# Optimization experiments

Measured on AMD Instinct MI355X. Metric: run time of the kernel, lower is better.

## Reference

```python
import jax, jax.numpy as jnp
import numpy as np

V, E, H, A, B, S = 32000, 1024, 1024, 1024, 64, 512

def setup_inputs() -> dict:
    key = jax.random.key(0)
    ks = jax.random.split(key, 20)
    sc = lambda d: 1.0 / np.sqrt(d)
    return {
        "x": jax.random.randint(ks[0], (B,), 0, V),
        "encoder_outputs": jax.random.normal(ks[1], (S, B, H), jnp.float32),
        "h0": jax.random.normal(ks[2], (1, B, H), jnp.float32),
        "c0": jax.random.normal(ks[3], (1, B, H), jnp.float32),
        "Wa": jax.random.normal(ks[4], (A, H), jnp.float32) * sc(H),
        "b_wa": jnp.zeros((A,), jnp.float32),
        "Ua": jax.random.normal(ks[5], (A, H), jnp.float32) * sc(H),
        "b_ua": jnp.zeros((A,), jnp.float32),
        "va": jax.random.normal(ks[6], (1, A), jnp.float32) * sc(A),
        "b_va": jnp.zeros((1,), jnp.float32),
        "emb": jax.random.normal(ks[7], (V, E), jnp.float32) * 0.02,
        "W_ih": jax.random.normal(ks[8], (4 * H, E + H), jnp.float32) * sc(E + H),
        "W_hh": jax.random.normal(ks[9], (4 * H, H), jnp.float32) * sc(H),
        "b_ih": jnp.zeros((4 * H,), jnp.float32),
        "b_hh": jnp.zeros((4 * H,), jnp.float32),
        "W_clf": jax.random.normal(ks[10], (V, H), jnp.float32) * sc(H),
        "b_clf": jnp.zeros((V,), jnp.float32),
    }

def reference(x, encoder_outputs, h0, c0, Wa, b_wa, Ua, b_ua, va, b_va, emb,
              W_ih, W_hh, b_ih, b_hh, W_clf, b_clf):
    # Bahdanau additive attention: scores over time (axis 0)
    tmp1 = jnp.einsum('lbh,ah->lba', h0, Wa) + b_wa            # [1,B,A]
    tmp2 = jnp.einsum('sbh,ah->sba', encoder_outputs, Ua) + b_ua  # [S,B,A]
    scores = jnp.einsum('sba,oa->sbo', jnp.tanh(tmp1 + tmp2), va) + b_va  # [S,B,1]
    w = jax.nn.softmax(scores, axis=0)                          # softmax over S
    ctx = jnp.einsum('sb,sbh->bh', w[..., 0], encoder_outputs)  # [B,H]
    # embed token, concat with context
    inp = jnp.concatenate([emb[x], ctx], axis=-1)               # [B,E+H]
    # single LSTM step (PyTorch gate order i,f,g,o)
    gates = inp @ W_ih.T + b_ih + h0[0] @ W_hh.T + b_hh         # [B,4H]
    i, f, g, o = jnp.split(gates, 4, axis=-1)
    c1 = jax.nn.sigmoid(f) * c0[0] + jax.nn.sigmoid(i) * jnp.tanh(g)
    h1 = jax.nn.sigmoid(o) * jnp.tanh(c1)
    logits = h1 @ W_clf.T + b_clf                               # [B,V]
    return jax.nn.log_softmax(logits, axis=-1)[None]            # [1,B,V]
```

## Files before the change

kernel.cpp:

```cpp
#include <hip/hip_runtime.h>
#include <hip/hip_bf16.h>
#include <math.h>

typedef unsigned short u16;
typedef unsigned int u32;
typedef __attribute__((ext_vector_type(4))) float f32x4;
typedef __attribute__((ext_vector_type(8))) short s16x8;
typedef __attribute__((ext_vector_type(8))) unsigned short u16x8;

#define DEV __device__ __forceinline__


DEV u16 f2bf(float f) {
    union { float f; u32 u; } x{f};
    return (u16)((x.u + 0x7FFFu + ((x.u >> 16) & 1u)) >> 16);
}
DEV float bf2f(u16 h) {
    union { u32 u; float f; } x;
    x.u = ((u32)h) << 16;
    return x.f;
}
DEV float sigm(float x) { return 1.0f / (1.0f + __expf(-x)); }
DEV float tanh_f(float x) {
    float c = fminf(fmaxf(x, -9.0f), 9.0f);
    float e = __expf(2.0f * c);
    return (e - 1.0f) / (e + 1.0f);
}

#define GLL16(g, l) __builtin_amdgcn_global_load_lds( \
    (const __attribute__((address_space(1))) u32*)(g), \
    (__attribute__((address_space(3))) u32*)(l), 16, 0, 0)

__global__ __launch_bounds__(256) void kprepcvt(
    const float* __restrict__ enc, const float* __restrict__ Ua,
    const float* __restrict__ h0, u16* __restrict__ encbf,
    u16* __restrict__ Uabf, u16* __restrict__ h0bf, float* __restrict__ scores)
{
    int bid = blockIdx.x, t = threadIdx.x;
    if (bid < 16384) {
        int i = bid * 256 + t;
        float4 f0 = ((const float4*)enc)[i * 2];
        float4 f1 = ((const float4*)enc)[i * 2 + 1];
        u16x8 o = {f2bf(f0.x), f2bf(f0.y), f2bf(f0.z), f2bf(f0.w),
                   f2bf(f1.x), f2bf(f1.y), f2bf(f1.z), f2bf(f1.w)};
        ((u16x8*)encbf)[i] = o;
    } else if (bid < 16400) {
        int i = (bid - 16384) * 2048 + t * 8;
        *(float4*)(scores + i) = (float4){0.f, 0.f, 0.f, 0.f};
        *(float4*)(scores + i + 4) = (float4){0.f, 0.f, 0.f, 0.f};
    } else if (bid < 16912) {
        int i = (bid - 16400) * 256 + t;
        float4 f0 = ((const float4*)Ua)[i * 2];
        float4 f1 = ((const float4*)Ua)[i * 2 + 1];
        u16x8 o = {f2bf(f0.x), f2bf(f0.y), f2bf(f0.z), f2bf(f0.w),
                   f2bf(f1.x), f2bf(f1.y), f2bf(f1.z), f2bf(f1.w)};
        ((u16x8*)Uabf)[i] = o;
    } else {
        int i = (bid - 16912) * 256 + t;
        float4 f0 = ((const float4*)h0)[i * 2];
        float4 f1 = ((const float4*)h0)[i * 2 + 1];
        u16x8 o = {f2bf(f0.x), f2bf(f0.y), f2bf(f0.z), f2bf(f0.w),
                   f2bf(f1.x), f2bf(f1.y), f2bf(f1.z), f2bf(f1.w)};
        ((u16x8*)h0bf)[i] = o;
    }
}


template<int F0>
DEV void mmq(f32x4 (&acc)[8][4], const s16x8 (&af)[2][2], const s16x8 (&bfrag)[4][2]) {
#pragma unroll
    for (int f = 0; f < 2; f++)
#pragma unroll
        for (int j = 0; j < 4; j++) {
            acc[F0 + f][j] = __builtin_amdgcn_mfma_f32_16x16x32_bf16(af[f][0], bfrag[j][0], acc[F0 + f][j], 0, 0, 0);
            acc[F0 + f][j] = __builtin_amdgcn_mfma_f32_16x16x32_bf16(af[f][1], bfrag[j][1], acc[F0 + f][j], 0, 0, 0);
        }
}

__global__ __launch_bounds__(512, 1) void kscores256v2(
    const u16* __restrict__ encbf, const u16* __restrict__ Uabf,
    const float* __restrict__ tmp1c, const float* __restrict__ va,
    float* __restrict__ scores)
{
    __shared__ __align__(16) u16 shm[65536];

    int wg  = blockIdx.x;
    int lin = (wg & 7) * 64 + (wg >> 3);
    int mt  = lin >> 2, nt = lin & 3;

    int t = threadIdx.x;
    int wid = t >> 6, lane = t & 63;
    int wm = wid >> 2, wn = wid & 3;
    int lr = lane & 15, lg = lane >> 4;

    f32x4 acc[8][4];
#pragma unroll
    for (int i = 0; i < 8; i++)
#pragma unroll
        for (int j = 0; j < 4; j++) acc[i][j] = (f32x4){0.f, 0.f, 0.f, 0.f};

    int srow = t >> 3;
    int sq8  = ((t & 7) ^ (srow & 7)) * 8;
    const u16* asrcb = encbf + (size_t)(mt * 256 + srow) * 1024 + sq8;
    const u16* bsrcb = Uabf + (size_t)(nt * 256 + srow) * 1024 + sq8;

#define STG_A(SE, RB, KO) GLL16(asrcb + (size_t)(RB) * 1024 + (KO), shm + (SE) + (RB) * 64 + t * 8)
#define STG_B(SE, RB, KO) GLL16(bsrcb + (size_t)(RB) * 1024 + (KO), shm + (SE) + 16384 + (RB) * 64 + t * 8)

    const u16* Abase = shm + (wm * 128 + lr) * 64;
    const u16* Bbase = shm + 16384 + (wn * 64 + lr) * 64;
    int xor8 = (lr & 7) * 8;
    int o0 = (lg * 8) ^ xor8;
    int o1 = (32 + lg * 8) ^ xor8;

    s16x8 af[2][2], bfrag[4][2];

#define RD_A2(F0, AB) { \
    af[0][0] = *(const s16x8*)((AB) + (F0) * 1024 + o0); \
    af[0][1] = *(const s16x8*)((AB) + (F0) * 1024 + o1); \
    af[1][0] = *(const s16x8*)((AB) + (F0 + 1) * 1024 + o0); \
    af[1][1] = *(const s16x8*)((AB) + (F0 + 1) * 1024 + o1); }

#define MM(F0) \
    __builtin_amdgcn_s_setprio(1); \
    mmq<F0>(acc, af, bfrag); \
    __builtin_amdgcn_s_setprio(0);

#define BAR() \
    __builtin_amdgcn_s_barrier(); \
    __builtin_amdgcn_sched_barrier(0);

    STG_B(0, 0, 0);  STG_B(0, 64, 0);  STG_B(0, 128, 0); STG_B(0, 192, 0);
    STG_A(0, 0, 0);  STG_A(0, 128, 0); STG_A(0, 64, 0);  STG_A(0, 192, 0);
    STG_B(32768, 0, 64);  STG_B(32768, 64, 64);
    STG_B(32768, 128, 64); STG_B(32768, 192, 64);
    STG_A(32768, 0, 64);  STG_A(32768, 128, 64);
    asm volatile("s_waitcnt vmcnt(6)" ::: "memory");
    BAR();

#define TILE_BODY(T, SB, SBX, SAH, STP2, WC) { \
    int kA = (T) * 64 + 128; \
    int kH = (T) * 64 + 64; \
    const u16* Ab = Abase + (SB); \
    const u16* Bb = Bbase + (SB); \
     \
    if (SAH) { STG_A((SBX), 64, kH); STG_A((SBX), 192, kH); } \
    _Pragma("unroll") \
    for (int j = 0; j < 4; j++) { \
        bfrag[j][0] = *(const s16x8*)(Bb + j * 1024 + o0); \
        bfrag[j][1] = *(const s16x8*)(Bb + j * 1024 + o1); \
    } \
    RD_A2(0, Ab); \
    MM(0); \
    BAR();                       \
     \
    if (STP2) { STG_B((SB), 0, kA); STG_B((SB), 64, kA); } \
    RD_A2(2, Ab); \
    MM(2); \
    __builtin_amdgcn_sched_barrier(0); \
     \
    if (STP2) { STG_B((SB), 128, kA); STG_B((SB), 192, kA); } \
    RD_A2(4, Ab); \
    MM(4); \
    BAR();                       \
     \
    if (STP2) { STG_A((SB), 0, kA); STG_A((SB), 128, kA); } \
    RD_A2(6, Ab); \
    if ((WC) == 6) { asm volatile("s_waitcnt vmcnt(6)" ::: "memory"); } \
    else if ((WC) == 0) { asm volatile("s_waitcnt vmcnt(0)" ::: "memory"); } \
    MM(6); \
    BAR();                       \
}

    for (int tt = 0; tt < 7; tt++) {
        int T0 = tt * 2;
        TILE_BODY(T0, 0, 32768, 1, 1, 6);
        TILE_BODY(T0 + 1, 32768, 0, 1, 1, 6);
    }
    TILE_BODY(14, 0, 32768, 1, 0, 0);
    TILE_BODY(15, 32768, 0, 0, 0, -1);

    float* ltmp = (float*)shm;
#pragma unroll
    for (int i = 0; i < 8; i++) {
        int idx = t + i * 512;
        int row = idx >> 6, c4 = idx & 63;
        float4 v = *(const float4*)(tmp1c + row * 1024 + nt * 256 + c4 * 4);
        *(float4*)(ltmp + row * 260 + c4 * 4) = v;
    }
    __syncthreads();

    float vaj[4];
#pragma unroll
    for (int j = 0; j < 4; j++) vaj[j] = va[nt * 256 + wn * 64 + j * 16 + lr];

#pragma unroll
    for (int fi = 0; fi < 8; fi++) {
        float rs[4] = {0.f, 0.f, 0.f, 0.f};
#pragma unroll
        for (int j = 0; j < 4; j++) {
            int ac = wn * 64 + j * 16 + lr;
#pragma unroll
            for (int r = 0; r < 4; r++) {
                int b = (fi * 16 + lg * 4 + r) & 63;
                rs[r] += vaj[j] * tanh_f(acc[fi][j][r] + ltmp[b * 260 + ac]);
            }
        }
#pragma unroll
        for (int m = 1; m < 16; m <<= 1)
#pragma unroll
            for (int r = 0; r < 4; r++) rs[r] += __shfl_xor(rs[r], m, 64);
        if (lr == 0) {
            int mrow = mt * 256 + wm * 128 + fi * 16 + lg * 4;
#pragma unroll
            for (int r = 0; r < 4; r++) atomicAdd(&scores[mrow + r], rs[r]);
        }
    }
#undef STG_A
#undef STG_B
#undef RD_A2
#undef MM
#undef BAR
#undef TILE_BODY
}

__global__ __launch_bounds__(256) void kskinny(
    const u16* __restrict__ Abf, int Ktot,
    const float* __restrict__ B1, int K1,
    const float* __restrict__ B2,
    float* __restrict__ Cout, int N, int klen)
{
    __shared__ u16 As[64 * 40];
    __shared__ u16 Bs[128 * 40];

    int nt = blockIdx.x, p = blockIdx.y;
    int t = threadIdx.x;
    int wid = t >> 6, lane = t & 63;
    int lr = lane & 15, lg = lane >> 4;
    int K2 = Ktot - K1;

    f32x4 acc[4][2];
#pragma unroll
    for (int i = 0; i < 4; i++)
#pragma unroll
        for (int j = 0; j < 2; j++) acc[i][j] = (f32x4){0.f, 0.f, 0.f, 0.f};

    int arow = t >> 2, aq = t & 3;
    const u16* ap = Abf + (size_t)arow * Ktot + aq * 8;
    u16* asw = &As[arow * 40 + aq * 8];

    int brow = t >> 1, bhalf = t & 1;
    int n = nt * 128 + brow;
    u16* bsw = &Bs[brow * 40 + bhalf * 16];

    int kbeg = p * klen, kend = kbeg + klen;
    for (int k0 = kbeg; k0 < kend; k0 += 32) {
        __syncthreads();
        *(uint4*)asw = *(const uint4*)(ap + k0);
        int kk = k0 + bhalf * 16;
        const float* bp = (kk < K1) ? (B1 + (size_t)n * K1 + kk)
                                    : (B2 + (size_t)n * K2 + (kk - K1));
        float4 b0 = ((const float4*)bp)[0];
        float4 b1 = ((const float4*)bp)[1];
        float4 b2 = ((const float4*)bp)[2];
        float4 b3 = ((const float4*)bp)[3];
        u16x8 q0 = {f2bf(b0.x), f2bf(b0.y), f2bf(b0.z), f2bf(b0.w),
                    f2bf(b1.x), f2bf(b1.y), f2bf(b1.z), f2bf(b1.w)};
        u16x8 q1 = {f2bf(b2.x), f2bf(b2.y), f2bf(b2.z), f2bf(b2.w),
                    f2bf(b3.x), f2bf(b3.y), f2bf(b3.z), f2bf(b3.w)};
        *(u16x8*)bsw = q0;
        *(u16x8*)(bsw + 8) = q1;
        __syncthreads();

        const u16* abase = &As[lr * 40 + lg * 8];
        const u16* bbase = &Bs[(wid * 32 + lr) * 40 + lg * 8];
        s16x8 af[4], bfr[2];
#pragma unroll
        for (int i = 0; i < 4; i++) af[i]  = *(const s16x8*)(abase + i * 16 * 40);
#pragma unroll
        for (int j = 0; j < 2; j++) bfr[j] = *(const s16x8*)(bbase + j * 16 * 40);
#pragma unroll
        for (int i = 0; i < 4; i++)
#pragma unroll
            for (int j = 0; j < 2; j++)
                acc[i][j] = __builtin_amdgcn_mfma_f32_16x16x32_bf16(af[i], bfr[j], acc[i][j], 0, 0, 0);
    }

#pragma unroll
    for (int i = 0; i < 4; i++)
#pragma unroll
        for (int j = 0; j < 2; j++) {
            int m = i * 16 + lg * 4;
            int col = nt * 128 + wid * 32 + j * 16 + lr;
#pragma unroll
            for (int r = 0; r < 4; r++)
                Cout[((size_t)(p * 64 + m + r)) * N + col] = acc[i][j][r];
        }
}

__global__ void kredbias(const float* __restrict__ part, const float* __restrict__ bias1,
                         const float* __restrict__ bias2, float* __restrict__ out,
                         int N, int P)
{
    int idx = blockIdx.x * blockDim.x + threadIdx.x;
    if (idx >= 64 * N) return;
    int n = idx % N;
    float v = bias1[n] + bias2[n];
    for (int p = 0; p < P; p++) v += part[(size_t)p * 64 * N + idx];
    out[idx] = v;
}

__global__ __launch_bounds__(256) void kctx(const u16* __restrict__ encbf,
                                            const float* __restrict__ scores,
                                            float* __restrict__ pctx)
{
    int b = blockIdx.x & 63, ch = blockIdx.x >> 6;
    int t = threadIdx.x;
    int lane = t & 63, wv = t >> 6;
    __shared__ float redm[4], reds[4];
    __shared__ float wch[64];

    float v0 = scores[(2 * t) * 64 + b];
    float v1 = scores[(2 * t + 1) * 64 + b];
    float m = fmaxf(v0, v1);
#pragma unroll
    for (int mask = 1; mask < 64; mask <<= 1) m = fmaxf(m, __shfl_xor(m, mask, 64));
    if (lane == 0) redm[wv] = m;
    __syncthreads();
    m = fmaxf(fmaxf(redm[0], redm[1]), fmaxf(redm[2], redm[3]));
    float e0 = __expf(v0 - m), e1 = __expf(v1 - m);
    float sum = e0 + e1;
#pragma unroll
    for (int mask = 1; mask < 64; mask <<= 1) sum += __shfl_xor(sum, mask, 64);
    if (lane == 0) reds[wv] = sum;
    __syncthreads();
    sum = (reds[0] + reds[1]) + (reds[2] + reds[3]);
    float inv = 1.0f / sum;
    int base = ch * 32;
    if (t >= base && t < base + 32) {
        wch[2 * (t - base)]     = e0 * inv;
        wch[2 * (t - base) + 1] = e1 * inv;
    }
    __syncthreads();

    float4 acc = {0.f, 0.f, 0.f, 0.f};
    int s0 = ch * 64;
#pragma unroll 4
    for (int si = 0; si < 64; si++) {
        int s = s0 + si;
        float wv2 = wch[si];
        ushort4 e = ((const ushort4*)(encbf + ((size_t)(s * 64 + b)) * 1024))[t];
        acc.x += wv2 * bf2f(e.x); acc.y += wv2 * bf2f(e.y);
        acc.z += wv2 * bf2f(e.z); acc.w += wv2 * bf2f(e.w);
    }
    ((float4*)pctx)[((size_t)(ch * 64 + b)) * 256 + t] = acc;
}

__global__ void kbuild(const int* __restrict__ x, const float* __restrict__ emb,
                       const float* __restrict__ pctx, const float* __restrict__ h0,
                       u16* __restrict__ inp2bf)
{
    int idx = blockIdx.x * blockDim.x + threadIdx.x;
    if (idx >= 64 * 3072) return;
    int b = idx / 3072, k = idx % 3072;
    float v;
    if (k < 1024) {
        v = emb[(size_t)x[b] * 1024 + k];
    } else if (k < 2048) {
        int h = k - 1024;
        v = 0.f;
        for (int p = 0; p < 8; p++) v += pctx[(size_t)(p * 64 + b) * 1024 + h];
    } else {
        v = h0[b * 1024 + (k - 2048)];
    }
    inp2bf[idx] = f2bf(v);
}

__global__ void klstm(const float* __restrict__ gp, const float* __restrict__ b_ih,
                      const float* __restrict__ b_hh, const float* __restrict__ c0,
                      u16* __restrict__ h1bf)
{
    int idx = blockIdx.x * blockDim.x + threadIdx.x;
    int b = idx >> 10, j = idx & 1023;
    float ig = b_ih[j] + b_hh[j];
    float fg = b_ih[1024 + j] + b_hh[1024 + j];
    float gg = b_ih[2048 + j] + b_hh[2048 + j];
    float og = b_ih[3072 + j] + b_hh[3072 + j];
    for (int p = 0; p < 8; p++) {
        const float* g = gp + ((size_t)p * 64 + b) * 4096;
        ig += g[j]; fg += g[1024 + j]; gg += g[2048 + j]; og += g[3072 + j];
    }
    float c = sigm(fg) * c0[idx] + sigm(ig) * tanh_f(gg);
    float h = sigm(og) * tanh_f(c);
    h1bf[idx] = f2bf(h);
}

__global__ __launch_bounds__(1024) void klogsoftmax(const float* __restrict__ lp,
                                                    const float* __restrict__ b_clf,
                                                    float* __restrict__ out)
{
    int b = blockIdx.x, t = threadIdx.x;
    __shared__ float red[16], red2[16];
    float v[32];
    float mx = -1e30f;
#pragma unroll
    for (int i = 0; i < 32; i++) {
        int idx = t + i * 1024;
        if (idx < 32000) {
            float s = b_clf[idx];
#pragma unroll
            for (int p = 0; p < 2; p++)
                s += lp[((size_t)(p * 64 + b)) * 32000 + idx];
            v[i] = s;
            mx = fmaxf(mx, v[i]);
        } else v[i] = -1e30f;
    }
#pragma unroll
    for (int mask = 1; mask < 64; mask <<= 1) mx = fmaxf(mx, __shfl_xor(mx, mask, 64));
    if ((t & 63) == 0) red[t >> 6] = mx;
    __syncthreads();
#pragma unroll
    for (int k = 0; k < 16; k++) mx = fmaxf(mx, red[k]);
    float s = 0.f;
#pragma unroll
    for (int i = 0; i < 32; i++) {
        int idx = t + i * 1024;
        if (idx < 32000) s += __expf(v[i] - mx);
    }
#pragma unroll
    for (int mask = 1; mask < 64; mask <<= 1) s += __shfl_xor(s, mask, 64);
    if ((t & 63) == 0) red2[t >> 6] = s;
    __syncthreads();
    s = 0.f;
#pragma unroll
    for (int k = 0; k < 16; k++) s += red2[k];
    float lse = mx + logf(s);
#pragma unroll
    for (int i = 0; i < 32; i++) {
        int idx = t + i * 1024;
        if (idx < 32000) out[(size_t)b * 32000 + idx] = v[i] - lse;
    }
}

extern "C" void kernel_launch(void* const* d_in, const int* in_sizes, int n_in,
                              void* d_out, int out_size, void* d_ws, size_t ws_size,
                              hipStream_t stream)
{
    const int*   x     = (const int*)d_in[0];
    const float* enc   = (const float*)d_in[1];
    const float* h0    = (const float*)d_in[2];
    const float* c0    = (const float*)d_in[3];
    const float* Wa    = (const float*)d_in[4];
    const float* b_wa  = (const float*)d_in[5];
    const float* Ua    = (const float*)d_in[6];
    const float* b_ua  = (const float*)d_in[7];
    const float* va    = (const float*)d_in[8];
    const float* emb   = (const float*)d_in[10];
    const float* W_ih  = (const float*)d_in[11];
    const float* W_hh  = (const float*)d_in[12];
    const float* b_ih  = (const float*)d_in[13];
    const float* b_hh  = (const float*)d_in[14];
    const float* W_clf = (const float*)d_in[15];
    const float* b_clf = (const float*)d_in[16];
    float* out = (float*)d_out;

    char* ws = (char*)d_ws;
    u16*   encbf    = (u16*)  (ws + 0);
    float* gparts   = (float*)(ws + 0);
    float* lparts   = (float*)(ws + 8388608);
    float* scores   = (float*)(ws + 67108864);
    float* tmp1part = (float*)(ws + 67371008);
    float* tmp1c    = (float*)(ws + 69468160);
    u16*   h0bf     = (u16*)  (ws + 69730304);
    u16*   Uabf     = (u16*)  (ws + 69861376);
    float* pctx     = (float*)(ws + 71958528);
    u16*   inp2bf   = (u16*)  (ws + 74055680);
    u16*   h1bf     = (u16*)  (ws + 74448896);

    kprepcvt<<<16944, 256, 0, stream>>>(enc, Ua, h0, encbf, Uabf, h0bf, scores);

    {
        dim3 g(8, 8);
        kskinny<<<g, 256, 0, stream>>>(h0bf, 1024, Wa, 1024, nullptr, tmp1part, 1024, 128);
    }
    kredbias<<<256, 256, 0, stream>>>(tmp1part, b_wa, b_ua, tmp1c, 1024, 8);

    kscores256v2<<<512, 512, 0, stream>>>(encbf, Uabf, tmp1c, va, scores);
    kctx<<<512, 256, 0, stream>>>(encbf, scores, pctx);
    kbuild<<<768, 256, 0, stream>>>(x, emb, pctx, h0, inp2bf);

    {
        dim3 g(32, 8);
        kskinny<<<g, 256, 0, stream>>>(inp2bf, 3072, W_ih, 2048, W_hh, gparts, 4096, 384);
    }
    klstm<<<256, 256, 0, stream>>>(gparts, b_ih, b_hh, c0, h1bf);

    {
        dim3 g(250, 2);
        kskinny<<<g, 256, 0, stream>>>(h1bf, 1024, W_clf, 1024, nullptr, lparts, 32000, 512);
    }
    klogsoftmax<<<64, 1024, 0, stream>>>(lparts, b_clf, out);
}
```

Measured before the change: 211.4 us.

## Split log-softmax into two-pass chunked kernels and widen context loads

The single 64-block log-softmax is replaced by two kernels over 512 blocks. The first computes per-chunk max and sum-exp and stores the bias-added logits, and the second combines the chunk statistics and writes the output. This fixes the low parallelism of 64 blocks on a large GPU, at the cost of one extra launch and an extra read and write of the logits. The context kernel now uses 128 threads, each loading 8 bf16 values per step instead of 4, for wider memory accesses.

```diff
diff --git a/kernel.cpp b/kernel.cpp
--- a/kernel.cpp
+++ b/kernel.cpp
@@ -310,50 +310,56 @@
     out[idx] = v;
 }
 
-__global__ __launch_bounds__(256) void kctx(const u16* __restrict__ encbf,
+__global__ __launch_bounds__(128) void kctx(const u16* __restrict__ encbf,
                                             const float* __restrict__ scores,
                                             float* __restrict__ pctx)
 {
     int b = blockIdx.x & 63, ch = blockIdx.x >> 6;
     int t = threadIdx.x;
     int lane = t & 63, wv = t >> 6;
-    __shared__ float redm[4], reds[4];
+    __shared__ float redm[2], reds[2];
     __shared__ float wch[64];
 
-    float v0 = scores[(2 * t) * 64 + b];
-    float v1 = scores[(2 * t + 1) * 64 + b];
-    float m = fmaxf(v0, v1);
+    float v[4];
+    float m = -1e30f;
+#pragma unroll
+    for (int k = 0; k < 4; k++) {
+        v[k] = scores[(t + k * 128) * 64 + b];
+        m = fmaxf(m, v[k]);
+    }
 #pragma unroll
     for (int mask = 1; mask < 64; mask <<= 1) m = fmaxf(m, __shfl_xor(m, mask, 64));
     if (lane == 0) redm[wv] = m;
     __syncthreads();
-    m = fmaxf(fmaxf(redm[0], redm[1]), fmaxf(redm[2], redm[3]));
-    float e0 = __expf(v0 - m), e1 = __expf(v1 - m);
-    float sum = e0 + e1;
+    m = fmaxf(redm[0], redm[1]);
+    float e[4], sum = 0.f;
+#pragma unroll
+    for (int k = 0; k < 4; k++) { e[k] = __expf(v[k] - m); sum += e[k]; }
 #pragma unroll
     for (int mask = 1; mask < 64; mask <<= 1) sum += __shfl_xor(sum, mask, 64);
     if (lane == 0) reds[wv] = sum;
     __syncthreads();
-    sum = (reds[0] + reds[1]) + (reds[2] + reds[3]);
+    sum = reds[0] + reds[1];
     float inv = 1.0f / sum;
-    int base = ch * 32;
-    if (t >= base && t < base + 32) {
-        wch[2 * (t - base)]     = e0 * inv;
-        wch[2 * (t - base) + 1] = e1 * inv;
+#pragma unroll
+    for (int k = 0; k < 4; k++) {
+        int s = t + k * 128;
+        if ((s >> 6) == ch) wch[s & 63] = e[k] * inv;
     }
     __syncthreads();
 
-    float4 acc = {0.f, 0.f, 0.f, 0.f};
+    float acc[8] = {0.f, 0.f, 0.f, 0.f, 0.f, 0.f, 0.f, 0.f};
     int s0 = ch * 64;
 #pragma unroll 4
     for (int si = 0; si < 64; si++) {
-        int s = s0 + si;
-        float wv2 = wch[si];
-        ushort4 e = ((const ushort4*)(encbf + ((size_t)(s * 64 + b)) * 1024))[t];
-        acc.x += wv2 * bf2f(e.x); acc.y += wv2 * bf2f(e.y);
-        acc.z += wv2 * bf2f(e.z); acc.w += wv2 * bf2f(e.w);
-    }
-    ((float4*)pctx)[((size_t)(ch * 64 + b)) * 256 + t] = acc;
+        float wvv = wch[si];
+        u16x8 ev = *(const u16x8*)(encbf + ((size_t)((s0 + si) * 64 + b)) * 1024 + t * 8);
+#pragma unroll
+        for (int k = 0; k < 8; k++) acc[k] += wvv * bf2f(ev[k]);
+    }
+    float* dst = pctx + ((size_t)(ch * 64 + b)) * 1024 + t * 8;
+    *(float4*)dst = (float4){acc[0], acc[1], acc[2], acc[3]};
+    *(float4*)(dst + 4) = (float4){acc[4], acc[5], acc[6], acc[7]};
 }
 
 __global__ void kbuild(const int* __restrict__ x, const float* __restrict__ emb,
@@ -395,50 +401,73 @@
     h1bf[idx] = f2bf(h);
 }
 
-__global__ __launch_bounds__(1024) void klogsoftmax(const float* __restrict__ lp,
-                                                    const float* __restrict__ b_clf,
-                                                    float* __restrict__ out)
-{
-    int b = blockIdx.x, t = threadIdx.x;
-    __shared__ float red[16], red2[16];
-    float v[32];
+__global__ __launch_bounds__(256) void klsm1(const float* __restrict__ lp,
+                                             const float* __restrict__ b_clf,
+                                             float* __restrict__ logitsc,
+                                             float* __restrict__ mp,
+                                             float* __restrict__ sp)
+{
+    int b = blockIdx.x >> 3, ch = blockIdx.x & 7;
+    int t = threadIdx.x;
+    int lane = t & 63, wv = t >> 6;
+    __shared__ float rm[4], rs[4];
+    size_t base = (size_t)b * 32000 + ch * 4000;
+    int vbase = ch * 4000;
+
+    float v[16];
     float mx = -1e30f;
 #pragma unroll
-    for (int i = 0; i < 32; i++) {
-        int idx = t + i * 1024;
-        if (idx < 32000) {
-            float s = b_clf[idx];
-#pragma unroll
-            for (int p = 0; p < 2; p++)
-                s += lp[((size_t)(p * 64 + b)) * 32000 + idx];
+    for (int i = 0; i < 16; i++) {
+        int idx = t + i * 256;
+        if (idx < 4000) {
+            float s = b_clf[vbase + idx] + lp[base + idx] + lp[2048000 + base + idx];
             v[i] = s;
-            mx = fmaxf(mx, v[i]);
+            mx = fmaxf(mx, s);
         } else v[i] = -1e30f;
     }
 #pragma unroll
     for (int mask = 1; mask < 64; mask <<= 1) mx = fmaxf(mx, __shfl_xor(mx, mask, 64));
-    if ((t & 63) == 0) red[t >> 6] = mx;
+    if (lane == 0) rm[wv] = mx;
     __syncthreads();
-#pragma unroll
-    for (int k = 0; k < 16; k++) mx = fmaxf(mx, red[k]);
+    mx = fmaxf(fmaxf(rm[0], rm[1]), fmaxf(rm[2], rm[3]));
     float s = 0.f;
 #pragma unroll
-    for (int i = 0; i < 32; i++) {
-        int idx = t + i * 1024;
-        if (idx < 32000) s += __expf(v[i] - mx);
+    for (int i = 0; i < 16; i++) {
+        int idx = t + i * 256;
+        if (idx < 4000) {
+            s += __expf(v[i] - mx);
+            logitsc[base + idx] = v[i];
+        }
     }
 #pragma unroll
     for (int mask = 1; mask < 64; mask <<= 1) s += __shfl_xor(s, mask, 64);
-    if ((t & 63) == 0) red2[t >> 6] = s;
+    if (lane == 0) rs[wv] = s;
     __syncthreads();
-    s = 0.f;
-#pragma unroll
-    for (int k = 0; k < 16; k++) s += red2[k];
-    float lse = mx + logf(s);
-#pragma unroll
-    for (int i = 0; i < 32; i++) {
-        int idx = t + i * 1024;
-        if (idx < 32000) out[(size_t)b * 32000 + idx] = v[i] - lse;
+    if (t == 0) {
+        mp[blockIdx.x] = mx;
+        sp[blockIdx.x] = (rs[0] + rs[1]) + (rs[2] + rs[3]);
+    }
+}
+
+__global__ __launch_bounds__(256) void klsm2(const float* __restrict__ logitsc,
+                                             const float* __restrict__ mp,
+                                             const float* __restrict__ sp,
+                                             float* __restrict__ out)
+{
+    int b = blockIdx.x >> 3, ch = blockIdx.x & 7;
+    int t = threadIdx.x;
+    float m = -1e30f;
+#pragma unroll
+    for (int k = 0; k < 8; k++) m = fmaxf(m, mp[b * 8 + k]);
+    float s = 0.f;
+#pragma unroll
+    for (int k = 0; k < 8; k++) s += sp[b * 8 + k] * __expf(mp[b * 8 + k] - m);
+    float lse = m + logf(s);
+    size_t base = (size_t)b * 32000 + ch * 4000;
+#pragma unroll
+    for (int i = 0; i < 16; i++) {
+        int idx = t + i * 256;
+        if (idx < 4000) out[base + idx] = logitsc[base + idx] - lse;
     }
 }
 
@@ -468,6 +497,7 @@
     u16*   encbf    = (u16*)  (ws + 0);
     float* gparts   = (float*)(ws + 0);
     float* lparts   = (float*)(ws + 8388608);
+    float* logitsc  = (float*)(ws + 25165824);
     float* scores   = (float*)(ws + 67108864);
     float* tmp1part = (float*)(ws + 67371008);
     float* tmp1c    = (float*)(ws + 69468160);
@@ -476,6 +506,8 @@
     float* pctx     = (float*)(ws + 71958528);
     u16*   inp2bf   = (u16*)  (ws + 74055680);
     u16*   h1bf     = (u16*)  (ws + 74448896);
+    float* mp       = (float*)(ws + 74579968);
+    float* sp       = (float*)(ws + 74582016);
 
     kprepcvt<<<16944, 256, 0, stream>>>(enc, Ua, h0, encbf, Uabf, h0bf, scores);
 
@@ -486,7 +518,7 @@
     kredbias<<<256, 256, 0, stream>>>(tmp1part, b_wa, b_ua, tmp1c, 1024, 8);
 
     kscores256v2<<<512, 512, 0, stream>>>(encbf, Uabf, tmp1c, va, scores);
-    kctx<<<512, 256, 0, stream>>>(encbf, scores, pctx);
+    kctx<<<512, 128, 0, stream>>>(encbf, scores, pctx);
     kbuild<<<768, 256, 0, stream>>>(x, emb, pctx, h0, inp2bf);
 
     {
@@ -499,5 +531,6 @@
         dim3 g(250, 2);
         kskinny<<<g, 256, 0, stream>>>(h1bf, 1024, W_clf, 1024, nullptr, lparts, 32000, 512);
     }
-    klogsoftmax<<<64, 1024, 0, stream>>>(lparts, b_clf, out);
-}
+    klsm1<<<512, 256, 0, stream>>>(lparts, b_clf, logitsc, mp, sp);
+    klsm2<<<512, 256, 0, stream>>>(logitsc, mp, sp, out);
+}
```

New measurement: 212.6 us. No clear change (+0.5%).

## Load Ua B-fragments directly from global memory instead of staging through LDS

Applied to the files above, without the earlier changes.

The scores GEMM kernel no longer stages the Ua (B) operand tiles through shared memory. Each wave now reads its B fragments straight from global/L2 into registers, while the encoder (A) operand keeps its LDS double buffering. This roughly halves LDS use and removes B staging traffic and some barrier phases. In exchange, B reads are uncoalesced per-lane global loads that may stall the MFMA loop, since Ua is reused across all 64 M-tiles mostly through cache.

```diff
diff --git a/kernel.cpp b/kernel.cpp
--- a/kernel.cpp
+++ b/kernel.cpp
@@ -77,12 +77,12 @@
         }
 }
 
-__global__ __launch_bounds__(512, 1) void kscores256v2(
+__global__ __launch_bounds__(512, 1) void kscores256v3(
     const u16* __restrict__ encbf, const u16* __restrict__ Uabf,
     const float* __restrict__ tmp1c, const float* __restrict__ va,
     float* __restrict__ scores)
 {
-    __shared__ __align__(16) u16 shm[65536];
+    __shared__ __align__(16) u16 shm[33280];
 
     int wg  = blockIdx.x;
     int lin = (wg & 7) * 64 + (wg >> 3);
@@ -102,16 +102,15 @@
     int srow = t >> 3;
     int sq8  = ((t & 7) ^ (srow & 7)) * 8;
     const u16* asrcb = encbf + (size_t)(mt * 256 + srow) * 1024 + sq8;
-    const u16* bsrcb = Uabf + (size_t)(nt * 256 + srow) * 1024 + sq8;
 
 #define STG_A(SE, RB, KO) GLL16(asrcb + (size_t)(RB) * 1024 + (KO), shm + (SE) + (RB) * 64 + t * 8)
-#define STG_B(SE, RB, KO) GLL16(bsrcb + (size_t)(RB) * 1024 + (KO), shm + (SE) + 16384 + (RB) * 64 + t * 8)
 
     const u16* Abase = shm + (wm * 128 + lr) * 64;
-    const u16* Bbase = shm + 16384 + (wn * 64 + lr) * 64;
     int xor8 = (lr & 7) * 8;
     int o0 = (lg * 8) ^ xor8;
     int o1 = (32 + lg * 8) ^ xor8;
+
+    const u16* browbase = Uabf + (size_t)(nt * 256 + wn * 64 + lr) * 1024 + lg * 8;
 
     s16x8 af[2][2], bfrag[4][2];
 
@@ -121,6 +120,15 @@
     af[1][0] = *(const s16x8*)((AB) + (F0 + 1) * 1024 + o0); \
     af[1][1] = *(const s16x8*)((AB) + (F0 + 1) * 1024 + o1); }
 
+#define LD_B(KT) { \
+    const u16* bp = browbase + (KT); \
+    _Pragma("unroll") \
+    for (int j = 0; j < 4; j++) { \
+        bfrag[j][0] = *(const s16x8*)(bp + (size_t)j * 16384); \
+        bfrag[j][1] = *(const s16x8*)(bp + (size_t)j * 16384 + 32); \
+    } \
+}
+
 #define MM(F0) \
     __builtin_amdgcn_s_setprio(1); \
     mmq<F0>(acc, af, bfrag); \
@@ -130,43 +138,33 @@
     __builtin_amdgcn_s_barrier(); \
     __builtin_amdgcn_sched_barrier(0);
 
-    STG_B(0, 0, 0);  STG_B(0, 64, 0);  STG_B(0, 128, 0); STG_B(0, 192, 0);
-    STG_A(0, 0, 0);  STG_A(0, 128, 0); STG_A(0, 64, 0);  STG_A(0, 192, 0);
-    STG_B(32768, 0, 64);  STG_B(32768, 64, 64);
-    STG_B(32768, 128, 64); STG_B(32768, 192, 64);
-    STG_A(32768, 0, 64);  STG_A(32768, 128, 64);
-    asm volatile("s_waitcnt vmcnt(6)" ::: "memory");
+    STG_A(0, 0, 0); STG_A(0, 128, 0); STG_A(0, 64, 0); STG_A(0, 192, 0);
+    STG_A(16384, 0, 64); STG_A(16384, 128, 64);
+    asm volatile("s_waitcnt vmcnt(2)" ::: "memory");
     BAR();
 
 #define TILE_BODY(T, SB, SBX, SAH, STP2, WC) { \
-    int kA = (T) * 64 + 128; \
-    int kH = (T) * 64 + 64; \
+    int kT = (T) * 64; \
     const u16* Ab = Abase + (SB); \
-    const u16* Bb = Bbase + (SB); \
      \
-    if (SAH) { STG_A((SBX), 64, kH); STG_A((SBX), 192, kH); } \
-    _Pragma("unroll") \
-    for (int j = 0; j < 4; j++) { \
-        bfrag[j][0] = *(const s16x8*)(Bb + j * 1024 + o0); \
-        bfrag[j][1] = *(const s16x8*)(Bb + j * 1024 + o1); \
-    } \
+    LD_B(kT); \
+    __builtin_amdgcn_sched_barrier(0); \
+    if (SAH) { STG_A((SBX), 64, kT + 64); STG_A((SBX), 192, kT + 64); } \
     RD_A2(0, Ab); \
     MM(0); \
+    __builtin_amdgcn_sched_barrier(0); \
+     \
+    RD_A2(2, Ab); \
+    MM(2); \
     BAR();                       \
      \
-    if (STP2) { STG_B((SB), 0, kA); STG_B((SB), 64, kA); } \
-    RD_A2(2, Ab); \
-    MM(2); \
+    if (STP2) { STG_A((SB), 0, kT + 128); STG_A((SB), 128, kT + 128); } \
+    RD_A2(4, Ab); \
+    MM(4); \
     __builtin_amdgcn_sched_barrier(0); \
      \
-    if (STP2) { STG_B((SB), 128, kA); STG_B((SB), 192, kA); } \
-    RD_A2(4, Ab); \
-    MM(4); \
-    BAR();                       \
-     \
-    if (STP2) { STG_A((SB), 0, kA); STG_A((SB), 128, kA); } \
     RD_A2(6, Ab); \
-    if ((WC) == 6) { asm volatile("s_waitcnt vmcnt(6)" ::: "memory"); } \
+    if ((WC) == 2) { asm volatile("s_waitcnt vmcnt(2)" ::: "memory"); } \
     else if ((WC) == 0) { asm volatile("s_waitcnt vmcnt(0)" ::: "memory"); } \
     MM(6); \
     BAR();                       \
@@ -174,11 +172,15 @@
 
     for (int tt = 0; tt < 7; tt++) {
         int T0 = tt * 2;
-        TILE_BODY(T0, 0, 32768, 1, 1, 6);
-        TILE_BODY(T0 + 1, 32768, 0, 1, 1, 6);
-    }
-    TILE_BODY(14, 0, 32768, 1, 0, 0);
-    TILE_BODY(15, 32768, 0, 0, 0, -1);
+        TILE_BODY(T0, 0, 16384, 1, 1, 2);
+        TILE_BODY(T0 + 1, 16384, 0, 1, 1, 2);
+    }
+    TILE_BODY(14, 0, 16384, 1, 0, 0);
+    TILE_BODY(15, 16384, 0, 0, 0, -1);
+
+    asm volatile("s_waitcnt vmcnt(0)" ::: "memory");
+    __builtin_amdgcn_s_barrier();
+    __builtin_amdgcn_sched_barrier(0);
 
     float* ltmp = (float*)shm;
 #pragma unroll
@@ -217,8 +219,8 @@
         }
     }
 #undef STG_A
-#undef STG_B
 #undef RD_A2
+#undef LD_B
 #undef MM
 #undef BAR
 #undef TILE_BODY
@@ -485,7 +487,7 @@
     }
     kredbias<<<256, 256, 0, stream>>>(tmp1part, b_wa, b_ua, tmp1c, 1024, 8);
 
-    kscores256v2<<<512, 512, 0, stream>>>(encbf, Uabf, tmp1c, va, scores);
+    kscores256v3<<<512, 512, 0, stream>>>(encbf, Uabf, tmp1c, va, scores);
     kctx<<<512, 256, 0, stream>>>(encbf, scores, pctx);
     kbuild<<<768, 256, 0, stream>>>(x, emb, pctx, h0, inp2bf);
 
```

Measured after the change: 256.6 us. 1.21x slower.
